# Kernel tuning notes

Measured on AMD Instinct MI355X. Metric: run time of the kernel, lower is better.

The kernel has to match this reference:

```python
import jax, jax.numpy as jnp
import numpy as np

D_MODEL = 1024
NUM_HEADS = 16
D_K = D_MODEL // NUM_HEADS  # 64
THETA = 10000.0


def setup_inputs() -> dict:
    key = jax.random.key(0)
    k_x, k_q, k_k, k_v, k_o = jax.random.split(key, 5)
    B, S = 2, 2048
    std = (2.0 / (D_MODEL + D_MODEL)) ** 0.5
    x = jax.random.normal(k_x, (B, S, D_MODEL), dtype=jnp.float32)
    Wq = std * jax.random.truncated_normal(k_q, -3.0, 3.0, (D_MODEL, D_MODEL), dtype=jnp.float32)
    Wk = std * jax.random.truncated_normal(k_k, -3.0, 3.0, (D_MODEL, D_MODEL), dtype=jnp.float32)
    Wv = std * jax.random.truncated_normal(k_v, -3.0, 3.0, (D_MODEL, D_MODEL), dtype=jnp.float32)
    Wo = std * jax.random.truncated_normal(k_o, -3.0, 3.0, (D_MODEL, D_MODEL), dtype=jnp.float32)
    return {"x": x, "Wq": Wq, "Wk": Wk, "Wv": Wv, "Wo": Wo}


def _apply_rope(t, cos, sin):
    # t: [B, H, S, d_k]; cos/sin: [S, d_k//2] broadcast over B, H
    tr = t.reshape(*t.shape[:-1], D_K // 2, 2)
    t1, t2 = tr[..., 0], tr[..., 1]
    r1 = t1 * cos - t2 * sin
    r2 = t1 * sin + t2 * cos
    return jnp.stack([r1, r2], axis=-1).reshape(t.shape)


def reference(x, Wq, Wk, Wv, Wo):
    B, S, D = x.shape
    H, dk = NUM_HEADS, D_K
    # projections (no bias): y = x @ W.T
    Q = (x @ Wq.T).reshape(B, S, H, dk).transpose(0, 2, 1, 3)  # [B,H,S,dk]
    K = (x @ Wk.T).reshape(B, S, H, dk).transpose(0, 2, 1, 3)
    V = (x @ Wv.T).reshape(B, S, H, dk).transpose(0, 2, 1, 3)
    # RoPE angles for positions 0..S-1
    pos = jnp.arange(S, dtype=jnp.float32)[:, None]            # [S,1]
    freqs = 1.0 / (THETA ** (jnp.arange(0, dk, 2, dtype=jnp.float32) / dk))  # [dk/2]
    angles = pos * freqs[None, :]                              # [S, dk/2]
    cos, sin = jnp.cos(angles), jnp.sin(angles)
    Q = _apply_rope(Q, cos, sin)
    K = _apply_rope(K, cos, sin)
    # causal scaled dot-product attention
    scores = jnp.einsum("bhqd,bhkd->bhqk", Q, K) / jnp.sqrt(jnp.float32(dk))
    causal = jnp.tril(jnp.ones((S, S), dtype=bool))
    scores = jnp.where(causal, scores, -jnp.inf)
    probs = jax.nn.softmax(scores, axis=-1)
    attn = jnp.einsum("bhqk,bhkd->bhqd", probs, V)             # [B,H,S,dk]
    attn = attn.transpose(0, 2, 1, 3).reshape(B, S, H * dk)
    return attn @ Wo.T
```

## Files before the change

kernel.cpp:

```cpp
#include <hip/hip_runtime.h>
#include <hip/hip_bf16.h>

typedef __bf16 bf16;
typedef __bf16 bf16x8 __attribute__((ext_vector_type(8)));
typedef float f32x4 __attribute__((ext_vector_type(4)));
typedef _Float16 f16;
typedef _Float16 f16x2 __attribute__((ext_vector_type(2)));

#define MFMA16(A, B, C) __builtin_amdgcn_mfma_f32_16x16x32_bf16((A), (B), (C), 0, 0, 0)

static __device__ __forceinline__ void gload16(const bf16* g, bf16* l) {
    __builtin_amdgcn_global_load_lds((const __attribute__((address_space(1))) void*)g,
                                     (__attribute__((address_space(3))) void*)l, 16, 0, 0);
}

__global__ void detect_kernel(const void* w, int* flag) {
    float v = (float)((const bf16*)w)[threadIdx.x];
    unsigned long long bad = __ballot(!(fabsf(v) < 1.0f));
    if (threadIdx.x == 0) *flag = bad ? 1 : 0;
}

__global__ __launch_bounds__(256) void convert_all(const void* x, const void* w0,
                                                   const void* w1, const void* w2,
                                                   const void* w3, bf16* xb, bf16* b0,
                                                   bf16* b1, bf16* b2, bf16* b3,
                                                   const int* flagp) {
    if (*flagp == 0) return;
    int id = (blockIdx.x * 256 + threadIdx.x) * 4;
    const int XN = 1 << 22;
    const float* src;
    bf16* dst;
    int off;
    if (id < XN) {
        src = (const float*)x; dst = xb; off = id;
    } else {
        int r = id - XN;
        int wi = r >> 20;
        off = r & ((1 << 20) - 1);
        src = (const float*)(wi == 0 ? w0 : wi == 1 ? w1 : wi == 2 ? w2 : w3);
        dst = (wi == 0 ? b0 : wi == 1 ? b1 : wi == 2 ? b2 : b3);
    }
    float4 v = *(const float4*)(src + off);
    bf16 o[4] = {(bf16)v.x, (bf16)v.y, (bf16)v.z, (bf16)v.w};
    *(uint2*)(dst + off) = *(uint2*)o;
}

template <int MODE>
__global__ __launch_bounds__(256, 3) void gemm_nt(const void* rawA, const bf16* convA,
                                                  const void* rW0, const bf16* cW0,
                                                  const void* rW1, const bf16* cW1,
                                                  const void* rW2, const bf16* cW2,
                                                  bf16* Qo, bf16* Ko, bf16* Vt,
                                                  bf16* p0, bf16* p1,
                                                  const int* flagp) {
    const int K = 1024;
    __shared__ __attribute__((aligned(16))) bf16 lsA[2][128 * 32];
    __shared__ __attribute__((aligned(16))) bf16 lsB[2][128 * 32];
    __shared__ __attribute__((aligned(8))) f16 ropeT[(MODE == 0) ? 8192 : 2];
    const int flag = *flagp;
    const bf16* A = flag ? convA : (const bf16*)rawA;
    int tensor, n0, m0, ks;
    const bf16* W;
    if (MODE == 0) {
        tensor = blockIdx.x >> 3;
        n0 = (blockIdx.x & 7) * 128;
        m0 = blockIdx.y * 128;
        ks = 0;
        W = tensor == 0 ? (flag ? cW0 : (const bf16*)rW0)
          : tensor == 1 ? (flag ? cW1 : (const bf16*)rW1)
                        : (flag ? cW2 : (const bf16*)rW2);
    } else {
        const int bid = blockIdx.x;
        ks = bid & 1;
        const int slot = bid >> 1;
        m0 = (slot & 31) * 128;
        n0 = (slot >> 5) * 128;
        tensor = 0;
        W = flag ? cW0 : (const bf16*)rW0;
    }
    const int t = threadIdx.x;
    const int w = t >> 6, lane = t & 63;
    const int wr = w >> 1, wc = w & 1;
    const int llo = lane & 15, quad = lane >> 4;
    const int sel = (llo >> 1) & 3;

    if constexpr (MODE == 0) {
#pragma unroll
        for (int i = 0; i < 16; ++i) {
            int e = t * 16 + i;
            int sloc = e >> 5, d2 = e & 31;
            int s = (m0 + sloc) & 2047;
            float freq = exp2f((float)d2 * -0.4152410118609203f);
            float rev = (float)s * freq * 0.15915494309189535f;
            rev -= floorf(rev);
            int sw = d2 ^ ((sloc & 3) << 3);
            ropeT[(sloc * 32 + sw) * 2] = (f16)__builtin_amdgcn_cosf(rev);
            ropeT[(sloc * 32 + sw) * 2 + 1] = (f16)__builtin_amdgcn_sinf(rev);
        }
    }

    f32x4 acc[4][4] = {};

    auto stage = [&](int k0, int buf) {
#pragma unroll
        for (int j = 0; j < 2; ++j) {
            int c = j * 256 + t;
            int row = c >> 2, pos = c & 3;
            int g = pos ^ ((row >> 1) & 3);
            gload16(A + (size_t)(m0 + row) * K + k0 + g * 8, &lsA[buf][c * 8]);
        }
#pragma unroll
        for (int j = 0; j < 2; ++j) {
            int c = j * 256 + t;
            int row = c >> 2, pos = c & 3;
            int g = pos ^ ((row >> 1) & 3);
            gload16(W + (size_t)(n0 + row) * K + k0 + g * 8, &lsB[buf][c * 8]);
        }
    };

    auto compute = [&](int buf) {
        bf16x8 a[4], bb[4];
#pragma unroll
        for (int mi = 0; mi < 4; ++mi) {
            int r = wr * 64 + mi * 16 + llo;
            a[mi] = *(const bf16x8*)&lsA[buf][r * 32 + ((quad ^ sel) * 8)];
        }
#pragma unroll
        for (int ni = 0; ni < 4; ++ni) {
            int r = wc * 64 + ni * 16 + llo;
            bb[ni] = *(const bf16x8*)&lsB[buf][r * 32 + ((quad ^ sel) * 8)];
        }
#pragma unroll
        for (int mi = 0; mi < 4; ++mi)
#pragma unroll
            for (int ni = 0; ni < 4; ++ni)
                acc[mi][ni] = MFMA16(a[mi], bb[ni], acc[mi][ni]);
    };

    const int kbase = (MODE == 1) ? ks * 512 : 0;
    const int NIT = (MODE == 1) ? 16 : 32;

    stage(kbase, 0);
    for (int it = 0; it < NIT; it += 2) {
        __syncthreads();
        stage(kbase + (it + 1) * 32, 1);
        compute(0);
        __syncthreads();
        if (it + 2 < NIT) stage(kbase + (it + 2) * 32, 0);
        compute(1);
    }

#pragma unroll
    for (int mi = 0; mi < 4; ++mi)
#pragma unroll
        for (int ni = 0; ni < 4; ++ni)
#pragma unroll
            for (int r = 0; r < 4; ++r) {
                int row = m0 + wr * 64 + mi * 16 + quad * 4 + r;
                int col = n0 + wc * 64 + ni * 16 + llo;
                float v = acc[mi][ni][r];
                if (MODE == 1) {
                    bf16* dst = ks ? p1 : p0;
                    dst[(size_t)row * 1024 + col] = (bf16)v;
                } else if (tensor == 2) {
                    int b = row >> 11, s = row & 2047;
                    Vt[((size_t)b * 1024 + col) * 2048 + s] = (bf16)v;
                } else {
                    int d = col & 63;
                    int sloc = wr * 64 + mi * 16 + quad * 4 + r;
                    int sw = (d >> 1) ^ ((sloc & 3) << 3);
                    float partner = __shfl_xor(v, 1);
                    f16x2 cp = *(const f16x2*)&ropeT[(sloc * 32 + sw) * 2];
                    float cs = (float)cp[0];
                    float sn = (float)cp[1];
                    float outv = v * cs + partner * sn * ((d & 1) ? 1.0f : -1.0f);
                    bf16* dst = (tensor == 0) ? Qo : Ko;
                    dst[(size_t)row * 1024 + col] = (bf16)outv;
                }
            }
}

__global__ __launch_bounds__(256) void reduce_out(const bf16* p0, const bf16* p1,
                                                  void* dout, const int* flagp) {
    int i = (blockIdx.x * 256 + threadIdx.x) * 8;
    bf16x8 a = *(const bf16x8*)(p0 + i);
    bf16x8 b = *(const bf16x8*)(p1 + i);
    float s[8];
#pragma unroll
    for (int j = 0; j < 8; ++j) s[j] = (float)a[j] + (float)b[j];
    if (*flagp) {
        float4 lo = {s[0], s[1], s[2], s[3]};
        float4 hi = {s[4], s[5], s[6], s[7]};
        *(float4*)((float*)dout + i) = lo;
        *(float4*)((float*)dout + i + 4) = hi;
    } else {
        bf16 o[8];
#pragma unroll
        for (int j = 0; j < 8; ++j) o[j] = (bf16)s[j];
        *(uint4*)((bf16*)dout + i) = *(uint4*)o;
    }
}

__global__ __launch_bounds__(256, 3) void attn_kernel(const bf16* __restrict__ Q,
                                                      const bf16* __restrict__ Kr,
                                                      const bf16* __restrict__ Vt,
                                                      bf16* __restrict__ O,
                                                      bf16* __restrict__ Opart,
                                                      float* __restrict__ lws) {
    __shared__ __attribute__((aligned(16))) bf16 lsK[2][64 * 64];
    __shared__ __attribute__((aligned(16))) bf16 lsV[2][64 * 64];
    __shared__ __attribute__((aligned(16))) bf16 lsP[4][32 * 64];
    const int blk = blockIdx.x;
    int ib, bh, s, tt0, tt1;
    bool split;
    if (blk < 512) {
        split = true;
        s = blk >> 8;
        int c = blk & 255;
        ib = 15 - (c >> 5);
        bh = c & 31;
        tt0 = s ? (ib + 1) : 0;
        tt1 = s ? (2 * ib + 1) : ib;
    } else {
        split = false;
        s = 0;
        int c = blk - 512;
        ib = c >> 5;
        bh = c & 31;
        tt0 = 0;
        tt1 = 2 * ib + 1;
    }
    const int b = bh >> 4, h = bh & 15;
    const int t = threadIdx.x, w = t >> 6, lane = t & 63;
    const int llo = lane & 15, quad = lane >> 4;
    const int q0w = ib * 128 + w * 32;

    bf16x8 aQ[2][2];
#pragma unroll
    for (int qi = 0; qi < 2; ++qi) {
        const size_t qb =
            ((size_t)(b * 2048 + q0w + qi * 16 + llo)) * 1024 + h * 64 + quad * 8;
        aQ[qi][0] = *(const bf16x8*)&Q[qb];
        aQ[qi][1] = *(const bf16x8*)&Q[qb + 32];
    }

    f32x4 o[2][4] = {};
    float lpart[2] = {0.f, 0.f};
    const float SC = 0.18033688011112042f;
    const int qlane0 = q0w + llo;

    const int srow8 = lane >> 3;
    const int sc = (lane & 7) ^ srow8;

    auto stage = [&](int tt, int buf) {
        const int kv0 = tt * 64;
#pragma unroll
        for (int jj = 0; jj < 2; ++jj) {
            int seg = w + jj * 4;
            int rowk = seg * 8 + srow8;
            gload16(&Kr[((size_t)(b * 2048 + kv0 + rowk)) * 1024 + h * 64 + sc * 8],
                    &lsK[buf][seg * 512 + lane * 8]);
            gload16(&Vt[((size_t)(b * 1024 + h * 64 + rowk)) * 2048 + kv0 + sc * 8],
                    &lsV[buf][seg * 512 + lane * 8]);
        }
    };

    stage(tt0, 0);

    for (int tt = tt0; tt <= tt1; ++tt) {
        const int cur = (tt - tt0) & 1;
        const int kv0 = tt * 64;
        __syncthreads();
        if (tt + 1 <= tt1) stage(tt + 1, cur ^ 1);

        if (kv0 <= q0w + 31) {
            bf16x8 kf[4][2];
#pragma unroll
            for (int half = 0; half < 4; ++half) {
                int rk = half * 16 + llo;
                kf[half][0] = *(const bf16x8*)&lsK[cur][rk * 64 + ((quad ^ (rk & 7)) * 8)];
                kf[half][1] =
                    *(const bf16x8*)&lsK[cur][rk * 64 + (((quad + 4) ^ (rk & 7)) * 8)];
            }
            bf16x8 vf[2][4];
#pragma unroll
            for (int kc = 0; kc < 2; ++kc)
#pragma unroll
                for (int g = 0; g < 4; ++g) {
                    int rv = g * 16 + llo;
                    int cg = kc * 4 + quad;
                    vf[kc][g] =
                        *(const bf16x8*)&lsV[cur][rv * 64 + ((cg ^ (rv & 7)) * 8)];
                }

            const bool need_mask = (kv0 + 63 >= q0w);
#pragma unroll
            for (int qi = 0; qi < 2; ++qi) {
                const int q = qlane0 + qi * 16;
                const int prow = qi * 16 + llo;
#pragma unroll
                for (int half = 0; half < 4; ++half) {
                    f32x4 z = {};
                    z = MFMA16(kf[half][0], aQ[qi][0], z);
                    z = MFMA16(kf[half][1], aQ[qi][1], z);
                    union { bf16 hh[4]; uint2 uu; } pk;
                    if (need_mask) {
                        int kvb = kv0 + half * 16 + quad * 4;
#pragma unroll
                        for (int r = 0; r < 4; ++r) {
                            float e = (kvb + r <= q) ? z[r] * SC : -INFINITY;
                            float p = __builtin_amdgcn_exp2f(e);
                            lpart[qi] += p;
                            pk.hh[r] = (bf16)p;
                        }
                    } else {
#pragma unroll
                        for (int r = 0; r < 4; ++r) {
                            float p = __builtin_amdgcn_exp2f(z[r] * SC);
                            lpart[qi] += p;
                            pk.hh[r] = (bf16)p;
                        }
                    }
                    int cw = 2 * half + (quad >> 1);
                    *(uint2*)&lsP[w][prow * 64 + ((cw ^ (llo & 7)) * 8) + (quad & 1) * 4] =
                        pk.uu;
                }
            }
            __builtin_amdgcn_wave_barrier();
#pragma unroll
            for (int qi = 0; qi < 2; ++qi) {
                const int prow = qi * 16 + llo;
#pragma unroll
                for (int kc = 0; kc < 2; ++kc) {
                    int cr = 4 * kc + quad;
                    bf16x8 aP =
                        *(const bf16x8*)&lsP[w][prow * 64 + ((cr ^ (llo & 7)) * 8)];
#pragma unroll
                    for (int g = 0; g < 4; ++g) o[qi][g] = MFMA16(aP, vf[kc][g], o[qi][g]);
                }
            }
            __builtin_amdgcn_wave_barrier();
        }
    }

    float lfull[2];
#pragma unroll
    for (int qi = 0; qi < 2; ++qi) {
        float l = lpart[qi];
        l += __shfl_xor(l, 16);
        l += __shfl_xor(l, 32);
        lfull[qi] = l;
    }

    if (split) {
        const int slotw = ((ib - 8) * 32 + bh) * 2 + s;
        bf16* op = Opart + (size_t)slotw * 8192;
#pragma unroll
        for (int qi = 0; qi < 2; ++qi) {
#pragma unroll
            for (int r = 0; r < 4; ++r) {
                int row_in = w * 32 + qi * 16 + quad * 4 + r;
#pragma unroll
                for (int g = 0; g < 4; ++g)
                    op[row_in * 64 + g * 16 + llo] = (bf16)o[qi][g][r];
            }
            if (quad == 0) lws[slotw * 128 + w * 32 + qi * 16 + llo] = lfull[qi];
        }
    } else {
#pragma unroll
        for (int qi = 0; qi < 2; ++qi)
#pragma unroll
            for (int r = 0; r < 4; ++r) {
                float l = __shfl(lfull[qi], (lane & 48) | (quad * 4 + r));
                float inv = 1.f / l;
                int q = q0w + qi * 16 + quad * 4 + r;
                size_t ob = ((size_t)(b * 2048 + q)) * 1024 + h * 64;
#pragma unroll
                for (int g = 0; g < 4; ++g)
                    O[ob + g * 16 + llo] = (bf16)(o[qi][g][r] * inv);
            }
    }
}

__global__ __launch_bounds__(256) void combine_kernel(const bf16* __restrict__ Opart,
                                                      const float* __restrict__ lws,
                                                      bf16* __restrict__ AO) {
    int vid = blockIdx.x * 256 + threadIdx.x;
    int d0 = (vid & 15) * 4;
    int h = (vid >> 4) & 15;
    int qoff = (vid >> 8) & 1023;
    int b = vid >> 18;
    int ib8 = qoff >> 7;
    int q_in = qoff & 127;
    int slot = (ib8 * 32 + (b * 16 + h)) * 2;
    size_t base = (size_t)slot * 8192 + q_in * 64 + d0;
    union { uint2 u; bf16 v[4]; } o0, o1, ov;
    o0.u = *(const uint2*)&Opart[base];
    o1.u = *(const uint2*)&Opart[base + 8192];
    float l = lws[slot * 128 + q_in] + lws[(slot + 1) * 128 + q_in];
    float inv = 1.f / l;
#pragma unroll
    for (int j = 0; j < 4; ++j) ov.v[j] = (bf16)(((float)o0.v[j] + (float)o1.v[j]) * inv);
    int q = 1024 + qoff;
    *(uint2*)&AO[((size_t)(b * 2048 + q)) * 1024 + h * 64 + d0] = ov.u;
}

extern "C" void kernel_launch(void* const* d_in, const int* in_sizes, int n_in,
                              void* d_out, int out_size, void* d_ws, size_t ws_size,
                              hipStream_t stream) {
    const size_t TN = (size_t)4096 * 1024;

    int* flag = (int*)d_ws;
    bf16* Q = (bf16*)((char*)d_ws + 256);
    bf16* Kb = Q + TN;
    bf16* Vt = Kb + TN;
    bf16* xb = Vt + TN;
    bf16* Wb0 = xb + TN;
    bf16* Wb1 = Wb0 + TN / 4;
    bf16* Wb2 = Wb1 + TN / 4;
    bf16* Wb3 = Wb2 + TN / 4;
    bf16* AO = Q;
    bf16* Opart = xb;
    float* lws = (float*)Wb0;
    bf16* p0 = Kb;
    bf16* p1 = xb;

    detect_kernel<<<1, 64, 0, stream>>>(d_in[1], flag);
    convert_all<<<8192, 256, 0, stream>>>(d_in[0], d_in[1], d_in[2], d_in[3], d_in[4],
                                          xb, Wb0, Wb1, Wb2, Wb3, flag);

    gemm_nt<0><<<dim3(24, 32), 256, 0, stream>>>(d_in[0], xb, d_in[1], Wb0, d_in[2],
                                                 Wb1, d_in[3], Wb2, Q, Kb, Vt, nullptr,
                                                 nullptr, flag);

    attn_kernel<<<768, 256, 0, stream>>>(Q, Kb, Vt, AO, Opart, lws);
    combine_kernel<<<2048, 256, 0, stream>>>(Opart, lws, AO);

    gemm_nt<1><<<512, 256, 0, stream>>>(AO, AO, d_in[4], Wb3, nullptr, nullptr,
                                        nullptr, nullptr, nullptr, nullptr, nullptr,
                                        p0, p1, flag);
    reduce_out<<<2048, 256, 0, stream>>>(p0, p1, d_out, flag);
}
```

Before: 195.3 us.

## Load K/V fragments directly from global, drop LDS staging; fold detect into convert

The attention kernel no longer stages K and V tiles into double-buffered shared memory with async global-to-LDS loads and block-wide barriers. Each wave now loads its own K and V fragments straight from global memory into registers and stops at its own causal limit. The separate detect kernel is merged into convert_all, which saves one launch. In exchange, the four waves of a block each fetch the same K/V data redundantly through the cache, and the loads are no longer prefetched one tile ahead, which risks exposed latency.

```diff
diff --git a/kernel.cpp b/kernel.cpp
--- a/kernel.cpp
+++ b/kernel.cpp
@@ -14,19 +14,23 @@
                                      (__attribute__((address_space(3))) void*)l, 16, 0, 0);
 }
 
-__global__ void detect_kernel(const void* w, int* flag) {
-    float v = (float)((const bf16*)w)[threadIdx.x];
-    unsigned long long bad = __ballot(!(fabsf(v) < 1.0f));
-    if (threadIdx.x == 0) *flag = bad ? 1 : 0;
-}
-
 __global__ __launch_bounds__(256) void convert_all(const void* x, const void* w0,
                                                    const void* w1, const void* w2,
                                                    const void* w3, bf16* xb, bf16* b0,
                                                    bf16* b1, bf16* b2, bf16* b3,
-                                                   const int* flagp) {
-    if (*flagp == 0) return;
-    int id = (blockIdx.x * 256 + threadIdx.x) * 4;
+                                                   int* flagp) {
+    __shared__ int sflag;
+    const int t = threadIdx.x;
+    if (t < 64) {
+        float v = (float)((const bf16*)w0)[t];
+        unsigned long long bad = __ballot(!(fabsf(v) < 1.0f));
+        if (t == 0) sflag = bad ? 1 : 0;
+    }
+    __syncthreads();
+    const int flag = sflag;
+    if (blockIdx.x == 0 && t == 0) *flagp = flag;
+    if (flag == 0) return;
+    int id = (blockIdx.x * 256 + t) * 4;
     const int XN = 1 << 22;
     const float* src;
     bf16* dst;
@@ -207,8 +211,6 @@
                                                       bf16* __restrict__ O,
                                                       bf16* __restrict__ Opart,
                                                       float* __restrict__ lws) {
-    __shared__ __attribute__((aligned(16))) bf16 lsK[2][64 * 64];
-    __shared__ __attribute__((aligned(16))) bf16 lsV[2][64 * 64];
     __shared__ __attribute__((aligned(16))) bf16 lsP[4][32 * 64];
     const int blk = blockIdx.x;
     int ib, bh, s, tt0, tt1;
@@ -249,98 +251,73 @@
     const float SC = 0.18033688011112042f;
     const int qlane0 = q0w + llo;
 
-    const int srow8 = lane >> 3;
-    const int sc = (lane & 7) ^ srow8;
-
-    auto stage = [&](int tt, int buf) {
+    const int tt1w = min(tt1, (q0w + 31) >> 6);
+
+    for (int tt = tt0; tt <= tt1w; ++tt) {
         const int kv0 = tt * 64;
-#pragma unroll
-        for (int jj = 0; jj < 2; ++jj) {
-            int seg = w + jj * 4;
-            int rowk = seg * 8 + srow8;
-            gload16(&Kr[((size_t)(b * 2048 + kv0 + rowk)) * 1024 + h * 64 + sc * 8],
-                    &lsK[buf][seg * 512 + lane * 8]);
-            gload16(&Vt[((size_t)(b * 1024 + h * 64 + rowk)) * 2048 + kv0 + sc * 8],
-                    &lsV[buf][seg * 512 + lane * 8]);
-        }
-    };
-
-    stage(tt0, 0);
-
-    for (int tt = tt0; tt <= tt1; ++tt) {
-        const int cur = (tt - tt0) & 1;
-        const int kv0 = tt * 64;
-        __syncthreads();
-        if (tt + 1 <= tt1) stage(tt + 1, cur ^ 1);
-
-        if (kv0 <= q0w + 31) {
-            bf16x8 kf[4][2];
+        bf16x8 kf[4][2];
+#pragma unroll
+        for (int half = 0; half < 4; ++half) {
+            const size_t kb =
+                ((size_t)(b * 2048 + kv0 + half * 16 + llo)) * 1024 + h * 64 + quad * 8;
+            kf[half][0] = *(const bf16x8*)&Kr[kb];
+            kf[half][1] = *(const bf16x8*)&Kr[kb + 32];
+        }
+        bf16x8 vf[2][4];
+#pragma unroll
+        for (int kc = 0; kc < 2; ++kc)
+#pragma unroll
+            for (int g = 0; g < 4; ++g)
+                vf[kc][g] = *(const bf16x8*)&Vt[((size_t)(b * 1024 + h * 64 + g * 16 +
+                                                          llo)) * 2048 +
+                                                kv0 + (kc * 4 + quad) * 8];
+
+        const bool need_mask = (kv0 + 63 >= q0w);
+#pragma unroll
+        for (int qi = 0; qi < 2; ++qi) {
+            const int q = qlane0 + qi * 16;
+            const int prow = qi * 16 + llo;
 #pragma unroll
             for (int half = 0; half < 4; ++half) {
-                int rk = half * 16 + llo;
-                kf[half][0] = *(const bf16x8*)&lsK[cur][rk * 64 + ((quad ^ (rk & 7)) * 8)];
-                kf[half][1] =
-                    *(const bf16x8*)&lsK[cur][rk * 64 + (((quad + 4) ^ (rk & 7)) * 8)];
+                f32x4 z = {};
+                z = MFMA16(kf[half][0], aQ[qi][0], z);
+                z = MFMA16(kf[half][1], aQ[qi][1], z);
+                union { bf16 hh[4]; uint2 uu; } pk;
+                if (need_mask) {
+                    int kvb = kv0 + half * 16 + quad * 4;
+#pragma unroll
+                    for (int r = 0; r < 4; ++r) {
+                        float e = (kvb + r <= q) ? z[r] * SC : -INFINITY;
+                        float p = __builtin_amdgcn_exp2f(e);
+                        lpart[qi] += p;
+                        pk.hh[r] = (bf16)p;
+                    }
+                } else {
+#pragma unroll
+                    for (int r = 0; r < 4; ++r) {
+                        float p = __builtin_amdgcn_exp2f(z[r] * SC);
+                        lpart[qi] += p;
+                        pk.hh[r] = (bf16)p;
+                    }
+                }
+                int cw = 2 * half + (quad >> 1);
+                *(uint2*)&lsP[w][prow * 64 + ((cw ^ (llo & 7)) * 8) + (quad & 1) * 4] =
+                    pk.uu;
             }
-            bf16x8 vf[2][4];
-#pragma unroll
-            for (int kc = 0; kc < 2; ++kc)
-#pragma unroll
-                for (int g = 0; g < 4; ++g) {
-                    int rv = g * 16 + llo;
-                    int cg = kc * 4 + quad;
-                    vf[kc][g] =
-                        *(const bf16x8*)&lsV[cur][rv * 64 + ((cg ^ (rv & 7)) * 8)];
-                }
-
-            const bool need_mask = (kv0 + 63 >= q0w);
-#pragma unroll
-            for (int qi = 0; qi < 2; ++qi) {
-                const int q = qlane0 + qi * 16;
-                const int prow = qi * 16 + llo;
-#pragma unroll
-                for (int half = 0; half < 4; ++half) {
-                    f32x4 z = {};
-                    z = MFMA16(kf[half][0], aQ[qi][0], z);
-                    z = MFMA16(kf[half][1], aQ[qi][1], z);
-                    union { bf16 hh[4]; uint2 uu; } pk;
-                    if (need_mask) {
-                        int kvb = kv0 + half * 16 + quad * 4;
-#pragma unroll
-                        for (int r = 0; r < 4; ++r) {
-                            float e = (kvb + r <= q) ? z[r] * SC : -INFINITY;
-                            float p = __builtin_amdgcn_exp2f(e);
-                            lpart[qi] += p;
-                            pk.hh[r] = (bf16)p;
-                        }
-                    } else {
-#pragma unroll
-                        for (int r = 0; r < 4; ++r) {
-                            float p = __builtin_amdgcn_exp2f(z[r] * SC);
-                            lpart[qi] += p;
-                            pk.hh[r] = (bf16)p;
-                        }
-                    }
-                    int cw = 2 * half + (quad >> 1);
-                    *(uint2*)&lsP[w][prow * 64 + ((cw ^ (llo & 7)) * 8) + (quad & 1) * 4] =
-                        pk.uu;
-                }
+        }
+        __builtin_amdgcn_wave_barrier();
+#pragma unroll
+        for (int qi = 0; qi < 2; ++qi) {
+            const int prow = qi * 16 + llo;
+#pragma unroll
+            for (int kc = 0; kc < 2; ++kc) {
+                int cr = 4 * kc + quad;
+                bf16x8 aP = *(const bf16x8*)&lsP[w][prow * 64 + ((cr ^ (llo & 7)) * 8)];
+#pragma unroll
+                for (int g = 0; g < 4; ++g) o[qi][g] = MFMA16(aP, vf[kc][g], o[qi][g]);
             }
-            __builtin_amdgcn_wave_barrier();
-#pragma unroll
-            for (int qi = 0; qi < 2; ++qi) {
-                const int prow = qi * 16 + llo;
-#pragma unroll
-                for (int kc = 0; kc < 2; ++kc) {
-                    int cr = 4 * kc + quad;
-                    bf16x8 aP =
-                        *(const bf16x8*)&lsP[w][prow * 64 + ((cr ^ (llo & 7)) * 8)];
-#pragma unroll
-                    for (int g = 0; g < 4; ++g) o[qi][g] = MFMA16(aP, vf[kc][g], o[qi][g]);
-                }
-            }
-            __builtin_amdgcn_wave_barrier();
-        }
+        }
+        __builtin_amdgcn_wave_barrier();
     }
 
     float lfull[2];
@@ -425,7 +402,6 @@
     bf16* p0 = Kb;
     bf16* p1 = xb;
 
-    detect_kernel<<<1, 64, 0, stream>>>(d_in[1], flag);
     convert_all<<<8192, 256, 0, stream>>>(d_in[0], d_in[1], d_in[2], d_in[3], d_in[4],
                                           xb, Wb0, Wb1, Wb2, Wb3, flag);
 
```

Result: slower. 221.0 us (+13.1%).
